# Kernel tuning notes

Measured on AMD Instinct MI355X. Metric: run time of the kernel, lower is better.

The kernel has to match this reference:

```python
import jax, jax.numpy as jnp
import numpy as np

B, N, D, L, T = 64, 64, 128, 4, 10  # batch, atoms, hidden_dim, n_layers, n_atom_types
EPS = 1e-5


def setup_inputs() -> dict:
    key = jax.random.key(0)
    ks = jax.random.split(key, 10)
    def rn(k, shape, s=0.05):
        return jax.random.normal(k, shape, jnp.float32) * s
    return dict(
        positions=jax.random.normal(ks[0], (B, N, 3), jnp.float32),
        atomic_numbers=jax.random.randint(ks[1], (B, N), 0, T),
        embed=rn(ks[2], (T, D)),
        edge_w1=rn(ks[3], (L, 2 * D + 1, D)), edge_b1=jnp.zeros((L, D), jnp.float32),
        edge_w2=rn(ks[4], (L, D, D)), edge_b2=jnp.zeros((L, D), jnp.float32),
        node_w1=rn(ks[5], (L, 2 * D, D)), node_b1=jnp.zeros((L, D), jnp.float32),
        node_w2=rn(ks[6], (L, D, D)), node_b2=jnp.zeros((L, D), jnp.float32),
        ln_g=jnp.ones((L, D), jnp.float32), ln_b=jnp.zeros((L, D), jnp.float32),
        out_w=rn(ks[7], (D, 3)), out_b=jnp.zeros((3,), jnp.float32),
    )


def _layer(h, dist_sq, ew1, eb1, ew2, eb2, nw1, nb1, nw2, nb2, g, b):
    # edge_mlp first linear on cat([h_i, h_j, dist_sq]) == h@Wa (bcast over j)
    # + h@Wb (bcast over i) + dist_sq * w_d, avoiding materializing the concat.
    wa, wb, wd = ew1[:D], ew1[D:2 * D], ew1[2 * D]
    pre = (h @ wa)[:, :, None, :] + (h @ wb)[:, None, :, :] + dist_sq * wd + eb1  # [B,N,N,D]
    m_ij = jax.nn.silu(jax.nn.silu(pre) @ ew2 + eb2)
    m_i = m_ij.mean(axis=2)  # mean over j -> [B,N,D]
    # node_mlp on cat([h, m_i]) split the same way; dropout is eval-mode identity.
    h_out = jax.nn.silu(h @ nw1[:D] + m_i @ nw1[D:] + nb1) @ nw2 + nb2
    x = h + h_out
    mu = x.mean(-1, keepdims=True)
    var = ((x - mu) ** 2).mean(-1, keepdims=True)
    return (x - mu) / jnp.sqrt(var + EPS) * g + b


def reference(positions, atomic_numbers, embed, edge_w1, edge_b1, edge_w2, edge_b2,
              node_w1, node_b1, node_w2, node_b2, ln_g, ln_b, out_w, out_b):
    h = embed[atomic_numbers]  # [B,N,D]
    diff = positions[:, :, None, :] - positions[:, None, :, :]
    dist_sq = (diff ** 2).sum(-1, keepdims=True)  # [B,N,N,1]
    for i in range(L):
        h = _layer(h, dist_sq, edge_w1[i], edge_b1[i], edge_w2[i], edge_b2[i],
                   node_w1[i], node_b1[i], node_w2[i], node_b2[i], ln_g[i], ln_b[i])
    return h @ out_w + out_b  # [B,N,3]
```

## Files before the change

kernel.cpp:

```cpp
#include <hip/hip_runtime.h>
#include <hip/hip_fp16.h>


typedef _Float16 f16;
typedef _Float16 f16x4 __attribute__((ext_vector_type(4)));
typedef _Float16 f16x8 __attribute__((ext_vector_type(8)));
typedef float f32x4 __attribute__((ext_vector_type(4)));

union H2x4 { f16x8 v; __half2 h[4]; };

__device__ __forceinline__ float bf2f(unsigned short u) {
    union { unsigned int i; float f; } v; v.i = ((unsigned int)u) << 16; return v.f;
}
__device__ __forceinline__ unsigned short f2bf(float f) {
    union { float f; unsigned int i; } v; v.f = f;
    unsigned int x = v.i;
    return (unsigned short)((x + 0x7fffu + ((x >> 16) & 1u)) >> 16);
}
__device__ __forceinline__ float silu_f(float x) {
    float e = __builtin_amdgcn_exp2f(-1.44269504088896f * x);
    return x * __builtin_amdgcn_rcpf(1.0f + e);
}
__device__ __forceinline__ __half2 silu_h2(__half2 x, __half2 kf, __half2 one2) {
    __half2 e = h2exp2(__hmul2(x, kf));
    return __hmul2(x, h2rcp(__hadd2(one2, e)));
}

struct Ptrs { const void* p[14]; };

__device__ __forceinline__ float ldf(const void* p, int i, int bf) {
    return bf ? bf2f(((const unsigned short*)p)[i]) : ((const float*)p)[i];
}

#define SWZ_TOTAL 393216
#define SMALL_TOTAL 17539

__global__ __launch_bounds__(256) void prep_kernel(
    Ptrs ptrs, f16* dst, float* sc)
{
    __shared__ int flgsh;
    int t = threadIdx.x;
    if (t < 64) {
        int ex = (((const unsigned short*)ptrs.p[0])[t * 2] >> 7) & 0xFF;
        unsigned long long m = __ballot(ex >= 110 && ex <= 135);
        if (t == 0) flgsh = (__popcll(m) >= 40) ? 1 : 0;
    }
    __syncthreads();
    int bf = flgsh;

    int gid = blockIdx.x * 256 + t;
    if (gid < SWZ_TOTAL) {
        int lay = gid / 98304;
        int r   = gid % 98304;
        const void* src; int base, rowoff = 0, r2;
        if (r < 49152) {
            int mat = r >> 14; r2 = r & 16383;
            if (mat == 0)      { src = ptrs.p[2]; base = lay * 32896; }
            else if (mat == 1) { src = ptrs.p[2]; base = lay * 32896; rowoff = 128; }
            else               { src = ptrs.p[4]; base = lay * 16384; }
        } else if (r < 81920) {
            r2 = r - 49152; src = ptrs.p[6]; base = lay * 32768;
        } else {
            r2 = r - 81920; src = ptrs.p[8]; base = lay * 16384;
        }
        int s = r2 >> 12, q = r2 & 4095;
        int j = q & 7, l = (q >> 3) & 63, c = q >> 9;
        int row = rowoff + s * 32 + ((l >> 4) << 3) + j;
        int col = (c << 4) + (l & 15);
        dst[gid] = (f16)ldf(src, base + row * 128 + col, bf);
    } else {
        int sid = gid - SWZ_TOTAL;
        if (sid >= SMALL_TOTAL) return;
        const void* src; int i;
        if      (sid < 12288) { src = ptrs.p[0]; i = sid; }
        else if (sid < 13568) { src = ptrs.p[1]; i = sid - 12288; }
        else if (sid < 14080) { int k = sid - 13568;
                                src = ptrs.p[2]; i = (k >> 7) * 32896 + 32768 + (k & 127); }
        else if (sid < 14592) { src = ptrs.p[3];  i = sid - 14080; }
        else if (sid < 15104) { src = ptrs.p[5];  i = sid - 14592; }
        else if (sid < 15616) { src = ptrs.p[7];  i = sid - 15104; }
        else if (sid < 16128) { src = ptrs.p[9];  i = sid - 15616; }
        else if (sid < 16640) { src = ptrs.p[10]; i = sid - 16128; }
        else if (sid < 17152) { src = ptrs.p[11]; i = sid - 16640; }
        else if (sid < 17536) { src = ptrs.p[12]; i = sid - 17152; }
        else                  { src = ptrs.p[13]; i = sid - 17536; }
        sc[sid] = ldf(src, i, bf);
    }
}

__global__ __launch_bounds__(256) void embed_ab_kernel(
    const int* an, const float* sc, const f16* wa, const f16* wb,
    const float* eb1C, f16* h16, f16* a16, f16* b16)
{
    int t = threadIdx.x;
    int w = t >> 6, lane = t & 63;
    int row0 = blockIdx.x << 4;
    int m_ = lane & 15, q_ = lane >> 4;
    const float* emb = sc + 12288;
    int a = an[row0 + m_];
    a = a < 0 ? 0 : (a > 9 ? 9 : a);
    f16x8 afrag[4];
#pragma unroll
    for (int s = 0; s < 4; s++) {
        f32x4 u0 = *(const f32x4*)(emb + a * 128 + s * 32 + q_ * 8);
        f32x4 u1 = *(const f32x4*)(emb + a * 128 + s * 32 + q_ * 8 + 4);
        f16x8 hv;
#pragma unroll
        for (int e = 0; e < 4; e++) { hv[e] = (f16)u0[e]; hv[e + 4] = (f16)u1[e]; }
        afrag[s] = hv;
        if (w == 0)
            *(f16x8*)(h16 + (row0 + m_) * 128 + s * 32 + q_ * 8) = hv;
    }
#pragma unroll
    for (int mat = 0; mat < 2; mat++) {
        const f16* W = mat ? wb : wa;
        f16* out     = mat ? b16 : a16;
#pragma unroll
        for (int cc = 0; cc < 2; cc++) {
            int c = 2 * w + cc;
            float init = mat ? 0.0f : eb1C[c * 16 + m_];
            f32x4 acc = { init, init, init, init };
#pragma unroll
            for (int s = 0; s < 4; s++) {
                f16x8 bfr = *(const f16x8*)(W + ((s * 8 + c) * 64 + lane) * 8);
                acc = __builtin_amdgcn_mfma_f32_16x16x32_f16(afrag[s], bfr, acc, 0, 0, 0);
            }
#pragma unroll
            for (int r = 0; r < 4; r++)
                out[(row0 + q_ * 4 + r) * 128 + c * 16 + m_] = (f16)acc[r];
        }
    }
}

__global__ __launch_bounds__(256) void edge_kernel(
    const float* sc, const f16* a16, const f16* b16,
    const f16* ew2_swz, const float* eb2C, const float* wdC, f16* m_out)
{
    __shared__ f16 Wlds[8192];
    __shared__ f16 S[64 * 136];
    __shared__ __half2 wd2_sh[64];
    __shared__ float dsq_sh[64];

    int t  = threadIdx.x;
    int ig = blockIdx.x;
    int b  = ig >> 6;
    const float* posC = sc;

#pragma unroll
    for (int k = 0; k < 4; k++) {
        int idx = (k * 256 + t) * 8;
        *(f16x8*)(Wlds + idx) = *(const f16x8*)(ew2_swz + idx);
    }
    if (t >= 64 && t < 128) {
        int u = t - 64;
        wd2_sh[u] = __floats2half2_rn(wdC[2 * u], wdC[2 * u + 1]);
    }
    if (t < 64) {
        float xi = posC[ig * 3 + 0], yi = posC[ig * 3 + 1], zi = posC[ig * 3 + 2];
        int jg = b * 64 + t;
        float dx = xi - posC[jg * 3 + 0];
        float dy = yi - posC[jg * 3 + 1];
        float dz = zi - posC[jg * 3 + 2];
        dsq_sh[t] = dx * dx + dy * dy + dz * dz;
    }
    __syncthreads();

    {
        int j  = t >> 2;
        int cb = (t & 3) * 32;
        float dsf = dsq_sh[j];
        __half dh = __float2half_rn(dsf);
        __half2 ds2 = __halves2half2(dh, dh);
        __half2 kf   = __floats2half2_rn(-1.44269504f, -1.44269504f);
        __half2 one2 = __floats2half2_rn(1.0f, 1.0f);
        H2x4 a_r[4], wd_r[4];
#pragma unroll
        for (int k = 0; k < 4; k++) {
            a_r[k].v  = *(const f16x8*)(a16 + ig * 128 + cb + k * 8);
            wd_r[k].v = *(const f16x8*)((const f16*)wd2_sh + cb + k * 8);
        }
#pragma unroll
        for (int k = 0; k < 4; k++) {
            H2x4 bv, sv;
            bv.v = *(const f16x8*)(b16 + (b * 64 + j) * 128 + cb + k * 8);
#pragma unroll
            for (int e = 0; e < 4; e++) {
                __half2 pre = __hfma2(ds2, wd_r[k].h[e],
                                      __hadd2(a_r[k].h[e], bv.h[e]));
                sv.h[e] = silu_h2(pre, kf, one2);
            }
            *(f16x8*)(S + j * 136 + cb + k * 8) = sv.v;
        }
    }
    __syncthreads();

    int lane = t & 63, w = t >> 6;
    int wr = w & 1, wc = w >> 1;
    int m_ = lane & 15, q_ = lane >> 4;
    f32x4 acc[4][2];
#pragma unroll
    for (int c = 0; c < 4; c++) {
        float e = eb2C[(wc * 4 + c) * 16 + m_];
        acc[c][0] = (f32x4){ e, e, e, e };
        acc[c][1] = (f32x4){ e, e, e, e };
    }
#pragma unroll
    for (int s = 0; s < 2; s++) {
        f16x8 bfr[4];
#pragma unroll
        for (int c = 0; c < 4; c++)
            bfr[c] = *(const f16x8*)(Wlds + ((s * 8 + wc * 4 + c) * 64 + lane) * 8);
#pragma unroll
        for (int mb = 0; mb < 2; mb++) {
            f16x8 af = *(const f16x8*)(S + ((wr * 2 + mb) * 16 + m_) * 136 + s * 32 + q_ * 8);
#pragma unroll
            for (int c = 0; c < 4; c++)
                acc[c][mb] = __builtin_amdgcn_mfma_f32_16x16x32_f16(af, bfr[c], acc[c][mb], 0, 0, 0);
        }
    }
    __syncthreads();
#pragma unroll
    for (int k = 0; k < 4; k++) {
        int idx = (k * 256 + t) * 8;
        *(f16x8*)(Wlds + idx) = *(const f16x8*)(ew2_swz + 8192 + idx);
    }
    __syncthreads();
#pragma unroll
    for (int s = 2; s < 4; s++) {
        f16x8 bfr[4];
#pragma unroll
        for (int c = 0; c < 4; c++)
            bfr[c] = *(const f16x8*)(Wlds + (((s - 2) * 8 + wc * 4 + c) * 64 + lane) * 8);
#pragma unroll
        for (int mb = 0; mb < 2; mb++) {
            f16x8 af = *(const f16x8*)(S + ((wr * 2 + mb) * 16 + m_) * 136 + s * 32 + q_ * 8);
#pragma unroll
            for (int c = 0; c < 4; c++)
                acc[c][mb] = __builtin_amdgcn_mfma_f32_16x16x32_f16(af, bfr[c], acc[c][mb], 0, 0, 0);
        }
    }
    float scv4[4];
#pragma unroll
    for (int c = 0; c < 4; c++) {
        float scv = 0.0f;
#pragma unroll
        for (int mb = 0; mb < 2; mb++)
#pragma unroll
            for (int r = 0; r < 4; r++)
                scv += silu_f(acc[c][mb][r]);
        scv += __shfl_xor(scv, 16);
        scv += __shfl_xor(scv, 32);
        scv4[c] = scv;
    }
    __syncthreads();
    float* msum = (float*)S;
    if (lane < 16) {
#pragma unroll
        for (int c = 0; c < 4; c++)
            msum[wr * 128 + (wc * 4 + c) * 16 + lane] = scv4[c];
    }
    __syncthreads();
    if (t < 128) {
        float mv = (msum[t] + msum[128 + t]) * (1.0f / 64.0f);
        m_out[ig * 128 + t] = (f16)mv;
    }
}

__global__ __launch_bounds__(256) void node_mid_kernel(
    const f16* h16, const f16* m16, const f16* nw1s, const f16* nw2s,
    const float* nb1C, const float* nb2C, const float* lngC, const float* lnbC,
    const f16* waN, const f16* wbN, const float* eb1N,
    f16* a16, f16* b16)
{
    __shared__ f16 relay[16 * 136];
    __shared__ float s1sh[4][16], s2sh[4][16];
    int t = threadIdx.x;
    int w = t >> 6, lane = t & 63;
    int row0 = blockIdx.x << 4;
    int m_ = lane & 15, q_ = lane >> 4;

    f16x8 af[8];
#pragma unroll
    for (int s = 0; s < 4; s++) {
        af[s]     = *(const f16x8*)(h16 + (row0 + m_) * 128 + s * 32 + q_ * 8);
        af[s + 4] = *(const f16x8*)(m16 + (row0 + m_) * 128 + s * 32 + q_ * 8);
    }
#pragma unroll
    for (int cc = 0; cc < 2; cc++) {
        int c = 2 * w + cc;
        float e = nb1C[c * 16 + m_];
        f32x4 acc = { e, e, e, e };
#pragma unroll
        for (int s = 0; s < 8; s++) {
            f16x8 bfr = *(const f16x8*)(nw1s + ((s * 8 + c) * 64 + lane) * 8);
            acc = __builtin_amdgcn_mfma_f32_16x16x32_f16(af[s], bfr, acc, 0, 0, 0);
        }
#pragma unroll
        for (int r = 0; r < 4; r++)
            relay[(q_ * 4 + r) * 136 + c * 16 + m_] = (f16)silu_f(acc[r]);
    }
    __syncthreads();
    f16x8 uf[4];
#pragma unroll
    for (int s = 0; s < 4; s++)
        uf[s] = *(const f16x8*)(relay + m_ * 136 + s * 32 + q_ * 8);
    float x[2][4];
#pragma unroll
    for (int cc = 0; cc < 2; cc++) {
        int c = 2 * w + cc;
        float e = nb2C[c * 16 + m_];
        f32x4 acc = { e, e, e, e };
#pragma unroll
        for (int s = 0; s < 4; s++) {
            f16x8 bfr = *(const f16x8*)(nw2s + ((s * 8 + c) * 64 + lane) * 8);
            acc = __builtin_amdgcn_mfma_f32_16x16x32_f16(uf[s], bfr, acc, 0, 0, 0);
        }
#pragma unroll
        for (int r = 0; r < 4; r++)
            x[cc][r] = acc[r] + (float)h16[(row0 + q_ * 4 + r) * 128 + c * 16 + m_];
    }
    float s1p[4], s2p[4];
#pragma unroll
    for (int r = 0; r < 4; r++) {
        s1p[r] = x[0][r] + x[1][r];
        s2p[r] = x[0][r] * x[0][r] + x[1][r] * x[1][r];
    }
#pragma unroll
    for (int msk = 1; msk < 16; msk <<= 1)
#pragma unroll
        for (int r = 0; r < 4; r++) {
            s1p[r] += __shfl_xor(s1p[r], msk);
            s2p[r] += __shfl_xor(s2p[r], msk);
        }
    if (m_ == 0)
#pragma unroll
        for (int r = 0; r < 4; r++) {
            s1sh[w][q_ * 4 + r] = s1p[r];
            s2sh[w][q_ * 4 + r] = s2p[r];
        }
    __syncthreads();
    float mu[4], rs[4];
#pragma unroll
    for (int r = 0; r < 4; r++) {
        int row = q_ * 4 + r;
        float S1 = s1sh[0][row] + s1sh[1][row] + s1sh[2][row] + s1sh[3][row];
        float S2 = s2sh[0][row] + s2sh[1][row] + s2sh[2][row] + s2sh[3][row];
        mu[r] = S1 * (1.0f / 128.0f);
        float var = S2 * (1.0f / 128.0f) - mu[r] * mu[r];
        rs[r] = rsqrtf(var + 1e-5f);
    }
#pragma unroll
    for (int cc = 0; cc < 2; cc++) {
        int c = 2 * w + cc;
#pragma unroll
        for (int r = 0; r < 4; r++) {
            int col = c * 16 + m_;
            int row = row0 + q_ * 4 + r;
            float y = (x[cc][r] - mu[r]) * rs[r] * lngC[col] + lnbC[col];
            ((f16*)h16)[row * 128 + col] = (f16)y;
            relay[(q_ * 4 + r) * 136 + col] = (f16)y;
        }
    }
    __syncthreads();
    f16x8 hf[4];
#pragma unroll
    for (int s = 0; s < 4; s++)
        hf[s] = *(const f16x8*)(relay + m_ * 136 + s * 32 + q_ * 8);
#pragma unroll
    for (int mat = 0; mat < 2; mat++) {
        const f16* W = mat ? wbN : waN;
        f16* out     = mat ? b16 : a16;
#pragma unroll
        for (int cc = 0; cc < 2; cc++) {
            int c = 2 * w + cc;
            float init = mat ? 0.0f : eb1N[c * 16 + m_];
            f32x4 acc = { init, init, init, init };
#pragma unroll
            for (int s = 0; s < 4; s++) {
                f16x8 bfr = *(const f16x8*)(W + ((s * 8 + c) * 64 + lane) * 8);
                acc = __builtin_amdgcn_mfma_f32_16x16x32_f16(hf[s], bfr, acc, 0, 0, 0);
            }
#pragma unroll
            for (int r = 0; r < 4; r++)
                out[(row0 + q_ * 4 + r) * 128 + c * 16 + m_] = (f16)acc[r];
        }
    }
}

__global__ __launch_bounds__(256) void node_final_kernel(
    const void* pos_raw, const f16* h16, const f16* m16,
    const f16* nw1s, const f16* nw2s,
    const float* nb1C, const float* nb2C, const float* lngC, const float* lnbC,
    const float* owC, const float* obC, void* out)
{
    __shared__ f16 relay[16 * 136];
    __shared__ float s1sh[4][16], s2sh[4][16];
    __shared__ float psh[4][16][3];
    __shared__ int flgsh;
    int t = threadIdx.x;
    int w = t >> 6, lane = t & 63;
    int row0 = blockIdx.x << 4;
    int m_ = lane & 15, q_ = lane >> 4;

    if (t < 64) {
        int ex = (((const unsigned short*)pos_raw)[t * 2] >> 7) & 0xFF;
        unsigned long long mk = __ballot(ex >= 110 && ex <= 135);
        if (t == 0) flgsh = (__popcll(mk) >= 40) ? 1 : 0;
    }

    f16x8 af[8];
#pragma unroll
    for (int s = 0; s < 4; s++) {
        af[s]     = *(const f16x8*)(h16 + (row0 + m_) * 128 + s * 32 + q_ * 8);
        af[s + 4] = *(const f16x8*)(m16 + (row0 + m_) * 128 + s * 32 + q_ * 8);
    }
#pragma unroll
    for (int cc = 0; cc < 2; cc++) {
        int c = 2 * w + cc;
        float e = nb1C[c * 16 + m_];
        f32x4 acc = { e, e, e, e };
#pragma unroll
        for (int s = 0; s < 8; s++) {
            f16x8 bfr = *(const f16x8*)(nw1s + ((s * 8 + c) * 64 + lane) * 8);
            acc = __builtin_amdgcn_mfma_f32_16x16x32_f16(af[s], bfr, acc, 0, 0, 0);
        }
#pragma unroll
        for (int r = 0; r < 4; r++)
            relay[(q_ * 4 + r) * 136 + c * 16 + m_] = (f16)silu_f(acc[r]);
    }
    __syncthreads();
    f16x8 uf[4];
#pragma unroll
    for (int s = 0; s < 4; s++)
        uf[s] = *(const f16x8*)(relay + m_ * 136 + s * 32 + q_ * 8);
    float x[2][4];
#pragma unroll
    for (int cc = 0; cc < 2; cc++) {
        int c = 2 * w + cc;
        float e = nb2C[c * 16 + m_];
        f32x4 acc = { e, e, e, e };
#pragma unroll
        for (int s = 0; s < 4; s++) {
            f16x8 bfr = *(const f16x8*)(nw2s + ((s * 8 + c) * 64 + lane) * 8);
            acc = __builtin_amdgcn_mfma_f32_16x16x32_f16(uf[s], bfr, acc, 0, 0, 0);
        }
#pragma unroll
        for (int r = 0; r < 4; r++)
            x[cc][r] = acc[r] + (float)h16[(row0 + q_ * 4 + r) * 128 + c * 16 + m_];
    }
    float s1p[4], s2p[4];
#pragma unroll
    for (int r = 0; r < 4; r++) {
        s1p[r] = x[0][r] + x[1][r];
        s2p[r] = x[0][r] * x[0][r] + x[1][r] * x[1][r];
    }
#pragma unroll
    for (int msk = 1; msk < 16; msk <<= 1)
#pragma unroll
        for (int r = 0; r < 4; r++) {
            s1p[r] += __shfl_xor(s1p[r], msk);
            s2p[r] += __shfl_xor(s2p[r], msk);
        }
    if (m_ == 0)
#pragma unroll
        for (int r = 0; r < 4; r++) {
            s1sh[w][q_ * 4 + r] = s1p[r];
            s2sh[w][q_ * 4 + r] = s2p[r];
        }
    __syncthreads();
    float p[3][4];
#pragma unroll
    for (int r = 0; r < 4; r++) {
        int row = q_ * 4 + r;
        float S1 = s1sh[0][row] + s1sh[1][row] + s1sh[2][row] + s1sh[3][row];
        float S2 = s2sh[0][row] + s2sh[1][row] + s2sh[2][row] + s2sh[3][row];
        float mu = S1 * (1.0f / 128.0f);
        float var = S2 * (1.0f / 128.0f) - mu * mu;
        float rs = rsqrtf(var + 1e-5f);
        float p0 = 0.0f, p1 = 0.0f, p2 = 0.0f;
#pragma unroll
        for (int cc = 0; cc < 2; cc++) {
            int col = (2 * w + cc) * 16 + m_;
            float y = (x[cc][r] - mu) * rs * lngC[col] + lnbC[col];
            p0 += y * owC[col * 3 + 0];
            p1 += y * owC[col * 3 + 1];
            p2 += y * owC[col * 3 + 2];
        }
        p[0][r] = p0; p[1][r] = p1; p[2][r] = p2;
    }
#pragma unroll
    for (int msk = 1; msk < 16; msk <<= 1)
#pragma unroll
        for (int k = 0; k < 3; k++)
#pragma unroll
            for (int r = 0; r < 4; r++)
                p[k][r] += __shfl_xor(p[k][r], msk);
    if (m_ == 0)
#pragma unroll
        for (int r = 0; r < 4; r++)
#pragma unroll
            for (int k = 0; k < 3; k++)
                psh[w][q_ * 4 + r][k] = p[k][r];
    __syncthreads();
    if (t < 16) {
        int row = row0 + t;
        int bf = flgsh;
#pragma unroll
        for (int k = 0; k < 3; k++) {
            float v = psh[0][t][k] + psh[1][t][k] + psh[2][t][k] + psh[3][t][k]
                      + obC[k];
            if (bf) ((unsigned short*)out)[row * 3 + k] = f2bf(v);
            else    ((float*)out)[row * 3 + k] = v;
        }
    }
}

extern "C" void kernel_launch(void* const* d_in, const int* in_sizes, int n_in,
                              void* d_out, int out_size, void* d_ws, size_t ws_size,
                              hipStream_t stream)
{
    const int* an = (const int*)d_in[1];

    char* ws = (char*)d_ws;
    float* sc   = (float*)(ws + 1024);
    f16*   Wswz = (f16*)(ws + (128u << 10));
    f16*   h16  = (f16*)(ws + (1u << 20));
    f16*   a16  = (f16*)(ws + (2u << 20));
    f16*   b16  = (f16*)(ws + (3u << 20));
    f16*   m16  = (f16*)(ws + (4u << 20));

    Ptrs ptrs;
    const int src_idx[14] = {0, 2, 3, 4, 5, 6, 7, 8, 9, 10, 11, 12, 13, 14};
    for (int k = 0; k < 14; k++) ptrs.p[k] = d_in[src_idx[k]];

    prep_kernel<<<1605, 256, 0, stream>>>(ptrs, Wswz, sc);
    embed_ab_kernel<<<256, 256, 0, stream>>>(an, sc, Wswz, Wswz + 16384,
                                             sc + 14080, h16, a16, b16);
    for (int lay = 0; lay < 4; lay++) {
        const f16* wl = Wswz + lay * 98304;
        const float* wdC  = sc + 13568 + lay * 128;
        const float* eb2C = sc + 14592 + lay * 128;
        const float* nb1C = sc + 15104 + lay * 128;
        const float* nb2C = sc + 15616 + lay * 128;
        const float* lngC = sc + 16128 + lay * 128;
        const float* lnbC = sc + 16640 + lay * 128;

        edge_kernel<<<4096, 256, 0, stream>>>(sc, a16, b16, wl + 32768,
                                              eb2C, wdC, m16);
        if (lay < 3) {
            const f16* wlN = Wswz + (lay + 1) * 98304;
            node_mid_kernel<<<256, 256, 0, stream>>>(
                h16, m16, wl + 49152, wl + 81920, nb1C, nb2C, lngC, lnbC,
                wlN, wlN + 16384, sc + 14080 + (lay + 1) * 128, a16, b16);
        } else {
            node_final_kernel<<<256, 256, 0, stream>>>(
                d_in[0], h16, m16, wl + 49152, wl + 81920,
                nb1C, nb2C, lngC, lnbC,
                sc + 17152, sc + 17536, d_out);
        }
    }
}
```

Measured before the change: 220.5 us.

## Process eight source atoms per edge block and keep full edge weight in LDS

The edge kernel now handles 8 i-atoms per block (512 blocks instead of 4096). It loads the whole 128x128 second edge weight into LDS once per block and keeps the b-row, j-position and bias values in registers across those 8 iterations, removing the repeated weight reloads and the mid-kernel refill barrier. The prep kernel also writes each swizzled fragment as one 8-wide f16 vector store per thread instead of scalar stores. In exchange, LDS use per block grows (about 52 KB) and there are fewer blocks, which can lower occupancy and latency hiding. Each i-iteration is serialized with two barriers.

```diff
diff --git a/kernel.cpp b/kernel.cpp
--- a/kernel.cpp
+++ b/kernel.cpp
@@ -32,7 +32,7 @@
     return bf ? bf2f(((const unsigned short*)p)[i]) : ((const float*)p)[i];
 }
 
-#define SWZ_TOTAL 393216
+#define FRAG_TOTAL 49152
 #define SMALL_TOTAL 17539
 
 __global__ __launch_bounds__(256) void prep_kernel(
@@ -49,27 +49,30 @@
     int bf = flgsh;
 
     int gid = blockIdx.x * 256 + t;
-    if (gid < SWZ_TOTAL) {
-        int lay = gid / 98304;
-        int r   = gid % 98304;
+    if (gid < FRAG_TOTAL) {
+        int lay = gid / 12288;
+        int r   = gid % 12288;
         const void* src; int base, rowoff = 0, r2;
-        if (r < 49152) {
-            int mat = r >> 14; r2 = r & 16383;
+        if (r < 6144) {
+            int mat = r >> 11; r2 = r & 2047;
             if (mat == 0)      { src = ptrs.p[2]; base = lay * 32896; }
             else if (mat == 1) { src = ptrs.p[2]; base = lay * 32896; rowoff = 128; }
             else               { src = ptrs.p[4]; base = lay * 16384; }
-        } else if (r < 81920) {
-            r2 = r - 49152; src = ptrs.p[6]; base = lay * 32768;
+        } else if (r < 10240) {
+            r2 = r - 6144; src = ptrs.p[6]; base = lay * 32768;
         } else {
-            r2 = r - 81920; src = ptrs.p[8]; base = lay * 16384;
-        }
-        int s = r2 >> 12, q = r2 & 4095;
-        int j = q & 7, l = (q >> 3) & 63, c = q >> 9;
-        int row = rowoff + s * 32 + ((l >> 4) << 3) + j;
-        int col = (c << 4) + (l & 15);
-        dst[gid] = (f16)ldf(src, base + row * 128 + col, bf);
+            r2 = r - 10240; src = ptrs.p[8]; base = lay * 16384;
+        }
+        int s = r2 >> 9, c = (r2 >> 6) & 7, l = r2 & 63;
+        int row0 = rowoff + s * 32 + ((l >> 4) << 3);
+        int col  = (c << 4) + (l & 15);
+        f16x8 v;
+#pragma unroll
+        for (int jj = 0; jj < 8; jj++)
+            v[jj] = (f16)ldf(src, base + (row0 + jj) * 128 + col, bf);
+        *(f16x8*)(dst + gid * 8) = v;
     } else {
-        int sid = gid - SWZ_TOTAL;
+        int sid = gid - FRAG_TOTAL;
         if (sid >= SMALL_TOTAL) return;
         const void* src; int i;
         if      (sid < 12288) { src = ptrs.p[0]; i = sid; }
@@ -136,18 +139,18 @@
     const float* sc, const f16* a16, const f16* b16,
     const f16* ew2_swz, const float* eb2C, const float* wdC, f16* m_out)
 {
-    __shared__ f16 Wlds[8192];
+    __shared__ f16 Wlds[16384];
     __shared__ f16 S[64 * 136];
+    __shared__ float msum[256];
     __shared__ __half2 wd2_sh[64];
-    __shared__ float dsq_sh[64];
-
-    int t  = threadIdx.x;
-    int ig = blockIdx.x;
-    int b  = ig >> 6;
+
+    int t   = threadIdx.x;
+    int ig0 = blockIdx.x * 8;
+    int b   = ig0 >> 6;
     const float* posC = sc;
 
 #pragma unroll
-    for (int k = 0; k < 4; k++) {
+    for (int k = 0; k < 8; k++) {
         int idx = (k * 256 + t) * 8;
         *(f16x8*)(Wlds + idx) = *(const f16x8*)(ew2_swz + idx);
     }
@@ -155,114 +158,89 @@
         int u = t - 64;
         wd2_sh[u] = __floats2half2_rn(wdC[2 * u], wdC[2 * u + 1]);
     }
-    if (t < 64) {
+
+    int j  = t >> 2;
+    int cb = (t & 3) * 32;
+    int jg = b * 64 + j;
+    float pxj = posC[jg * 3 + 0], pyj = posC[jg * 3 + 1], pzj = posC[jg * 3 + 2];
+    __half2 kf   = __floats2half2_rn(-1.44269504f, -1.44269504f);
+    __half2 one2 = __floats2half2_rn(1.0f, 1.0f);
+    H2x4 b_r[4];
+#pragma unroll
+    for (int k = 0; k < 4; k++)
+        b_r[k].v = *(const f16x8*)(b16 + jg * 128 + cb + k * 8);
+
+    int lane = t & 63, w = t >> 6;
+    int wr = w & 1, wc = w >> 1;
+    int m_ = lane & 15, q_ = lane >> 4;
+    float ebias[4];
+#pragma unroll
+    for (int c = 0; c < 4; c++) ebias[c] = eb2C[(wc * 4 + c) * 16 + m_];
+
+    __syncthreads();
+    H2x4 wd_r[4];
+#pragma unroll
+    for (int k = 0; k < 4; k++)
+        wd_r[k].v = *(const f16x8*)((const f16*)wd2_sh + cb + k * 8);
+
+    for (int ii = 0; ii < 8; ii++) {
+        int ig = ig0 + ii;
         float xi = posC[ig * 3 + 0], yi = posC[ig * 3 + 1], zi = posC[ig * 3 + 2];
-        int jg = b * 64 + t;
-        float dx = xi - posC[jg * 3 + 0];
-        float dy = yi - posC[jg * 3 + 1];
-        float dz = zi - posC[jg * 3 + 2];
-        dsq_sh[t] = dx * dx + dy * dy + dz * dz;
-    }
-    __syncthreads();
-
-    {
-        int j  = t >> 2;
-        int cb = (t & 3) * 32;
-        float dsf = dsq_sh[j];
-        __half dh = __float2half_rn(dsf);
+        float dx = xi - pxj, dy = yi - pyj, dz = zi - pzj;
+        __half dh = __float2half_rn(dx * dx + dy * dy + dz * dz);
         __half2 ds2 = __halves2half2(dh, dh);
-        __half2 kf   = __floats2half2_rn(-1.44269504f, -1.44269504f);
-        __half2 one2 = __floats2half2_rn(1.0f, 1.0f);
-        H2x4 a_r[4], wd_r[4];
 #pragma unroll
         for (int k = 0; k < 4; k++) {
-            a_r[k].v  = *(const f16x8*)(a16 + ig * 128 + cb + k * 8);
-            wd_r[k].v = *(const f16x8*)((const f16*)wd2_sh + cb + k * 8);
-        }
-#pragma unroll
-        for (int k = 0; k < 4; k++) {
-            H2x4 bv, sv;
-            bv.v = *(const f16x8*)(b16 + (b * 64 + j) * 128 + cb + k * 8);
+            H2x4 av, sv;
+            av.v = *(const f16x8*)(a16 + ig * 128 + cb + k * 8);
 #pragma unroll
             for (int e = 0; e < 4; e++) {
                 __half2 pre = __hfma2(ds2, wd_r[k].h[e],
-                                      __hadd2(a_r[k].h[e], bv.h[e]));
+                                      __hadd2(av.h[e], b_r[k].h[e]));
                 sv.h[e] = silu_h2(pre, kf, one2);
             }
             *(f16x8*)(S + j * 136 + cb + k * 8) = sv.v;
         }
-    }
-    __syncthreads();
-
-    int lane = t & 63, w = t >> 6;
-    int wr = w & 1, wc = w >> 1;
-    int m_ = lane & 15, q_ = lane >> 4;
-    f32x4 acc[4][2];
-#pragma unroll
-    for (int c = 0; c < 4; c++) {
-        float e = eb2C[(wc * 4 + c) * 16 + m_];
-        acc[c][0] = (f32x4){ e, e, e, e };
-        acc[c][1] = (f32x4){ e, e, e, e };
-    }
-#pragma unroll
-    for (int s = 0; s < 2; s++) {
-        f16x8 bfr[4];
-#pragma unroll
-        for (int c = 0; c < 4; c++)
-            bfr[c] = *(const f16x8*)(Wlds + ((s * 8 + wc * 4 + c) * 64 + lane) * 8);
-#pragma unroll
-        for (int mb = 0; mb < 2; mb++) {
-            f16x8 af = *(const f16x8*)(S + ((wr * 2 + mb) * 16 + m_) * 136 + s * 32 + q_ * 8);
+        __syncthreads();
+
+        f32x4 acc[4][2];
+#pragma unroll
+        for (int c = 0; c < 4; c++) {
+            acc[c][0] = (f32x4){ ebias[c], ebias[c], ebias[c], ebias[c] };
+            acc[c][1] = acc[c][0];
+        }
+#pragma unroll
+        for (int s = 0; s < 4; s++) {
+            f16x8 bfr[4];
 #pragma unroll
             for (int c = 0; c < 4; c++)
-                acc[c][mb] = __builtin_amdgcn_mfma_f32_16x16x32_f16(af, bfr[c], acc[c][mb], 0, 0, 0);
-        }
-    }
-    __syncthreads();
-#pragma unroll
-    for (int k = 0; k < 4; k++) {
-        int idx = (k * 256 + t) * 8;
-        *(f16x8*)(Wlds + idx) = *(const f16x8*)(ew2_swz + 8192 + idx);
-    }
-    __syncthreads();
-#pragma unroll
-    for (int s = 2; s < 4; s++) {
-        f16x8 bfr[4];
-#pragma unroll
-        for (int c = 0; c < 4; c++)
-            bfr[c] = *(const f16x8*)(Wlds + (((s - 2) * 8 + wc * 4 + c) * 64 + lane) * 8);
-#pragma unroll
-        for (int mb = 0; mb < 2; mb++) {
-            f16x8 af = *(const f16x8*)(S + ((wr * 2 + mb) * 16 + m_) * 136 + s * 32 + q_ * 8);
-#pragma unroll
-            for (int c = 0; c < 4; c++)
-                acc[c][mb] = __builtin_amdgcn_mfma_f32_16x16x32_f16(af, bfr[c], acc[c][mb], 0, 0, 0);
-        }
-    }
-    float scv4[4];
-#pragma unroll
-    for (int c = 0; c < 4; c++) {
-        float scv = 0.0f;
-#pragma unroll
-        for (int mb = 0; mb < 2; mb++)
-#pragma unroll
-            for (int r = 0; r < 4; r++)
-                scv += silu_f(acc[c][mb][r]);
-        scv += __shfl_xor(scv, 16);
-        scv += __shfl_xor(scv, 32);
-        scv4[c] = scv;
-    }
-    __syncthreads();
-    float* msum = (float*)S;
-    if (lane < 16) {
-#pragma unroll
-        for (int c = 0; c < 4; c++)
-            msum[wr * 128 + (wc * 4 + c) * 16 + lane] = scv4[c];
-    }
-    __syncthreads();
-    if (t < 128) {
-        float mv = (msum[t] + msum[128 + t]) * (1.0f / 64.0f);
-        m_out[ig * 128 + t] = (f16)mv;
+                bfr[c] = *(const f16x8*)(Wlds + ((s * 8 + wc * 4 + c) * 64 + lane) * 8);
+#pragma unroll
+            for (int mb = 0; mb < 2; mb++) {
+                f16x8 af = *(const f16x8*)(S + ((wr * 2 + mb) * 16 + m_) * 136 + s * 32 + q_ * 8);
+#pragma unroll
+                for (int c = 0; c < 4; c++)
+                    acc[c][mb] = __builtin_amdgcn_mfma_f32_16x16x32_f16(af, bfr[c], acc[c][mb], 0, 0, 0);
+            }
+        }
+#pragma unroll
+        for (int c = 0; c < 4; c++) {
+            float scv = 0.0f;
+#pragma unroll
+            for (int mb = 0; mb < 2; mb++)
+#pragma unroll
+                for (int r = 0; r < 4; r++)
+                    scv += silu_f(acc[c][mb][r]);
+            scv += __shfl_xor(scv, 16);
+            scv += __shfl_xor(scv, 32);
+            if (lane < 16)
+                msum[wr * 128 + (wc * 4 + c) * 16 + lane] = scv;
+        }
+        __syncthreads();
+        if (t < 128) {
+            float mv = (msum[t] + msum[128 + t]) * (1.0f / 64.0f);
+            m_out[ig * 128 + t] = (f16)mv;
+        }
     }
 }
 
@@ -533,7 +511,7 @@
     const int src_idx[14] = {0, 2, 3, 4, 5, 6, 7, 8, 9, 10, 11, 12, 13, 14};
     for (int k = 0; k < 14; k++) ptrs.p[k] = d_in[src_idx[k]];
 
-    prep_kernel<<<1605, 256, 0, stream>>>(ptrs, Wswz, sc);
+    prep_kernel<<<261, 256, 0, stream>>>(ptrs, Wswz, sc);
     embed_ab_kernel<<<256, 256, 0, stream>>>(an, sc, Wswz, Wswz + 16384,
                                              sc + 14080, h16, a16, b16);
     for (int lay = 0; lay < 4; lay++) {
@@ -545,8 +523,8 @@
         const float* lngC = sc + 16128 + lay * 128;
         const float* lnbC = sc + 16640 + lay * 128;
 
-        edge_kernel<<<4096, 256, 0, stream>>>(sc, a16, b16, wl + 32768,
-                                              eb2C, wdC, m16);
+        edge_kernel<<<512, 256, 0, stream>>>(sc, a16, b16, wl + 32768,
+                                             eb2C, wdC, m16);
         if (lay < 3) {
             const f16* wlN = Wswz + (lay + 1) * 98304;
             node_mid_kernel<<<256, 256, 0, stream>>>(
```

Result: slower. 234.1 us (+6.1%).

## Stream edge W2 weights in quarter chunks with register prefetch

Applied to the files above, without the earlier changes.

The edge kernel now keeps a quarter-size LDS weight buffer instead of a half-size one. It loads the next K-slice of the second edge-layer weights into registers while the MFMAs for the current slice run, then writes them to LDS between barriers. A separate msum buffer also removes one barrier before the reduction. The aim is to cut LDS usage so more blocks fit per CU, and to hide the global weight loads. The cost is more barriers per block, three sync pairs instead of one.

```diff
diff --git a/kernel.cpp b/kernel.cpp
--- a/kernel.cpp
+++ b/kernel.cpp
@@ -136,8 +136,9 @@
     const float* sc, const f16* a16, const f16* b16,
     const f16* ew2_swz, const float* eb2C, const float* wdC, f16* m_out)
 {
-    __shared__ f16 Wlds[8192];
+    __shared__ f16 Wlds[4096];
     __shared__ f16 S[64 * 136];
+    __shared__ float msum[256];
     __shared__ __half2 wd2_sh[64];
     __shared__ float dsq_sh[64];
 
@@ -147,7 +148,7 @@
     const float* posC = sc;
 
 #pragma unroll
-    for (int k = 0; k < 4; k++) {
+    for (int k = 0; k < 2; k++) {
         int idx = (k * 256 + t) * 8;
         *(f16x8*)(Wlds + idx) = *(const f16x8*)(ew2_swz + idx);
     }
@@ -202,14 +203,20 @@
     for (int c = 0; c < 4; c++) {
         float e = eb2C[(wc * 4 + c) * 16 + m_];
         acc[c][0] = (f32x4){ e, e, e, e };
-        acc[c][1] = (f32x4){ e, e, e, e };
-    }
-#pragma unroll
-    for (int s = 0; s < 2; s++) {
+        acc[c][1] = acc[c][0];
+    }
+#pragma unroll
+    for (int s = 0; s < 4; s++) {
+        f16x8 pf0, pf1;
+        if (s < 3) {
+            int base = (s + 1) * 4096;
+            pf0 = *(const f16x8*)(ew2_swz + base + t * 8);
+            pf1 = *(const f16x8*)(ew2_swz + base + 2048 + t * 8);
+        }
         f16x8 bfr[4];
 #pragma unroll
         for (int c = 0; c < 4; c++)
-            bfr[c] = *(const f16x8*)(Wlds + ((s * 8 + wc * 4 + c) * 64 + lane) * 8);
+            bfr[c] = *(const f16x8*)(Wlds + ((wc * 4 + c) * 64 + lane) * 8);
 #pragma unroll
         for (int mb = 0; mb < 2; mb++) {
             f16x8 af = *(const f16x8*)(S + ((wr * 2 + mb) * 16 + m_) * 136 + s * 32 + q_ * 8);
@@ -217,29 +224,13 @@
             for (int c = 0; c < 4; c++)
                 acc[c][mb] = __builtin_amdgcn_mfma_f32_16x16x32_f16(af, bfr[c], acc[c][mb], 0, 0, 0);
         }
-    }
-    __syncthreads();
-#pragma unroll
-    for (int k = 0; k < 4; k++) {
-        int idx = (k * 256 + t) * 8;
-        *(f16x8*)(Wlds + idx) = *(const f16x8*)(ew2_swz + 8192 + idx);
-    }
-    __syncthreads();
-#pragma unroll
-    for (int s = 2; s < 4; s++) {
-        f16x8 bfr[4];
-#pragma unroll
-        for (int c = 0; c < 4; c++)
-            bfr[c] = *(const f16x8*)(Wlds + (((s - 2) * 8 + wc * 4 + c) * 64 + lane) * 8);
-#pragma unroll
-        for (int mb = 0; mb < 2; mb++) {
-            f16x8 af = *(const f16x8*)(S + ((wr * 2 + mb) * 16 + m_) * 136 + s * 32 + q_ * 8);
-#pragma unroll
-            for (int c = 0; c < 4; c++)
-                acc[c][mb] = __builtin_amdgcn_mfma_f32_16x16x32_f16(af, bfr[c], acc[c][mb], 0, 0, 0);
-        }
-    }
-    float scv4[4];
+        if (s < 3) {
+            __syncthreads();
+            *(f16x8*)(Wlds + t * 8) = pf0;
+            *(f16x8*)(Wlds + 2048 + t * 8) = pf1;
+            __syncthreads();
+        }
+    }
 #pragma unroll
     for (int c = 0; c < 4; c++) {
         float scv = 0.0f;
@@ -250,14 +241,8 @@
                 scv += silu_f(acc[c][mb][r]);
         scv += __shfl_xor(scv, 16);
         scv += __shfl_xor(scv, 32);
-        scv4[c] = scv;
-    }
-    __syncthreads();
-    float* msum = (float*)S;
-    if (lane < 16) {
-#pragma unroll
-        for (int c = 0; c < 4; c++)
-            msum[wr * 128 + (wc * 4 + c) * 16 + lane] = scv4[c];
+        if (lane < 16)
+            msum[wr * 128 + (wc * 4 + c) * 16 + lane] = scv;
     }
     __syncthreads();
     if (t < 128) {
```

After: 223.7 us. About the same (+1.4%).

## Preload second-half edge weights into registers and vectorize weight prep

Applied to the files above, without the earlier changes.

The edge kernel now loads the second half of the W2 fragments straight from global memory into registers at kernel start, so the mid-kernel LDS reload and its two barriers go away and the load overlaps the SiLU stage. The prep kernel now has each thread write a packed 8-element f16 fragment instead of one element, cutting its grid from 1605 to 261 blocks. The cost is 32 more VGPRs held across the first stage, which may lower occupancy.

```diff
diff --git a/kernel.cpp b/kernel.cpp
--- a/kernel.cpp
+++ b/kernel.cpp
@@ -32,7 +32,7 @@
     return bf ? bf2f(((const unsigned short*)p)[i]) : ((const float*)p)[i];
 }
 
-#define SWZ_TOTAL 393216
+#define FRAG_TOTAL 49152
 #define SMALL_TOTAL 17539
 
 __global__ __launch_bounds__(256) void prep_kernel(
@@ -49,27 +49,30 @@
     int bf = flgsh;
 
     int gid = blockIdx.x * 256 + t;
-    if (gid < SWZ_TOTAL) {
-        int lay = gid / 98304;
-        int r   = gid % 98304;
+    if (gid < FRAG_TOTAL) {
+        int lay = gid / 12288;
+        int r   = gid % 12288;
         const void* src; int base, rowoff = 0, r2;
-        if (r < 49152) {
-            int mat = r >> 14; r2 = r & 16383;
+        if (r < 6144) {
+            int mat = r >> 11; r2 = r & 2047;
             if (mat == 0)      { src = ptrs.p[2]; base = lay * 32896; }
             else if (mat == 1) { src = ptrs.p[2]; base = lay * 32896; rowoff = 128; }
             else               { src = ptrs.p[4]; base = lay * 16384; }
-        } else if (r < 81920) {
-            r2 = r - 49152; src = ptrs.p[6]; base = lay * 32768;
+        } else if (r < 10240) {
+            r2 = r - 6144; src = ptrs.p[6]; base = lay * 32768;
         } else {
-            r2 = r - 81920; src = ptrs.p[8]; base = lay * 16384;
-        }
-        int s = r2 >> 12, q = r2 & 4095;
-        int j = q & 7, l = (q >> 3) & 63, c = q >> 9;
-        int row = rowoff + s * 32 + ((l >> 4) << 3) + j;
-        int col = (c << 4) + (l & 15);
-        dst[gid] = (f16)ldf(src, base + row * 128 + col, bf);
+            r2 = r - 10240; src = ptrs.p[8]; base = lay * 16384;
+        }
+        int s = r2 >> 9, c = (r2 >> 6) & 7, l = r2 & 63;
+        int row0 = rowoff + s * 32 + ((l >> 4) << 3);
+        int col  = (c << 4) + (l & 15);
+        f16x8 v;
+#pragma unroll
+        for (int jj = 0; jj < 8; jj++)
+            v[jj] = (f16)ldf(src, base + (row0 + jj) * 128 + col, bf);
+        *(f16x8*)(dst + gid * 8) = v;
     } else {
-        int sid = gid - SWZ_TOTAL;
+        int sid = gid - FRAG_TOTAL;
         if (sid >= SMALL_TOTAL) return;
         const void* src; int i;
         if      (sid < 12288) { src = ptrs.p[0]; i = sid; }
@@ -145,12 +148,22 @@
     int ig = blockIdx.x;
     int b  = ig >> 6;
     const float* posC = sc;
+    int lane = t & 63, w = t >> 6;
+    int wr = w & 1, wc = w >> 1;
 
 #pragma unroll
     for (int k = 0; k < 4; k++) {
         int idx = (k * 256 + t) * 8;
         *(f16x8*)(Wlds + idx) = *(const f16x8*)(ew2_swz + idx);
     }
+    f16x8 bfB[2][4];
+#pragma unroll
+    for (int s2 = 0; s2 < 2; s2++)
+#pragma unroll
+        for (int c = 0; c < 4; c++)
+            bfB[s2][c] = *(const f16x8*)(ew2_swz +
+                (((s2 + 2) * 8 + wc * 4 + c) * 64 + lane) * 8);
+
     if (t >= 64 && t < 128) {
         int u = t - 64;
         wd2_sh[u] = __floats2half2_rn(wdC[2 * u], wdC[2 * u + 1]);
@@ -194,15 +207,13 @@
     }
     __syncthreads();
 
-    int lane = t & 63, w = t >> 6;
-    int wr = w & 1, wc = w >> 1;
     int m_ = lane & 15, q_ = lane >> 4;
     f32x4 acc[4][2];
 #pragma unroll
     for (int c = 0; c < 4; c++) {
         float e = eb2C[(wc * 4 + c) * 16 + m_];
         acc[c][0] = (f32x4){ e, e, e, e };
-        acc[c][1] = (f32x4){ e, e, e, e };
+        acc[c][1] = acc[c][0];
     }
 #pragma unroll
     for (int s = 0; s < 2; s++) {
@@ -218,25 +229,14 @@
                 acc[c][mb] = __builtin_amdgcn_mfma_f32_16x16x32_f16(af, bfr[c], acc[c][mb], 0, 0, 0);
         }
     }
-    __syncthreads();
-#pragma unroll
-    for (int k = 0; k < 4; k++) {
-        int idx = (k * 256 + t) * 8;
-        *(f16x8*)(Wlds + idx) = *(const f16x8*)(ew2_swz + 8192 + idx);
-    }
-    __syncthreads();
-#pragma unroll
-    for (int s = 2; s < 4; s++) {
-        f16x8 bfr[4];
-#pragma unroll
-        for (int c = 0; c < 4; c++)
-            bfr[c] = *(const f16x8*)(Wlds + (((s - 2) * 8 + wc * 4 + c) * 64 + lane) * 8);
+#pragma unroll
+    for (int s2 = 0; s2 < 2; s2++) {
 #pragma unroll
         for (int mb = 0; mb < 2; mb++) {
-            f16x8 af = *(const f16x8*)(S + ((wr * 2 + mb) * 16 + m_) * 136 + s * 32 + q_ * 8);
+            f16x8 af = *(const f16x8*)(S + ((wr * 2 + mb) * 16 + m_) * 136 + (s2 + 2) * 32 + q_ * 8);
 #pragma unroll
             for (int c = 0; c < 4; c++)
-                acc[c][mb] = __builtin_amdgcn_mfma_f32_16x16x32_f16(af, bfr[c], acc[c][mb], 0, 0, 0);
+                acc[c][mb] = __builtin_amdgcn_mfma_f32_16x16x32_f16(af, bfB[s2][c], acc[c][mb], 0, 0, 0);
         }
     }
     float scv4[4];
@@ -533,7 +533,7 @@
     const int src_idx[14] = {0, 2, 3, 4, 5, 6, 7, 8, 9, 10, 11, 12, 13, 14};
     for (int k = 0; k < 14; k++) ptrs.p[k] = d_in[src_idx[k]];
 
-    prep_kernel<<<1605, 256, 0, stream>>>(ptrs, Wswz, sc);
+    prep_kernel<<<261, 256, 0, stream>>>(ptrs, Wswz, sc);
     embed_ab_kernel<<<256, 256, 0, stream>>>(an, sc, Wswz, Wswz + 16384,
                                              sc + 14080, h16, a16, b16);
     for (int lay = 0; lay < 4; lay++) {
```

Result: faster. 215.4 us (median of 2 runs) (-2.3%).
